# Optimization experiments

Measured on AMD Instinct MI355X. Metric: run time of the kernel, lower is better.

The kernel has to match this reference:

```python
import jax, jax.numpy as jnp
import numpy as np

B, PIX_H, PIX_W = 64, 14, 14
ENC_D, DEC_D, ATT_D, EMB_D = 2048, 512, 512, 512
VOCAB, MAX_LEN = 10000, 52  # 51 decode steps


def setup_inputs() -> dict:
    key = jax.random.key(0)
    ks = jax.random.split(key, 24)
    s = 0.02
    inp = {
        'encoder_out': jax.random.normal(ks[0], (B, PIX_H, PIX_W, ENC_D), jnp.float32),
        'encoded_captions': jax.random.randint(ks[1], (B, MAX_LEN), 0, VOCAB),
        'caption_lengths': jnp.sort(jax.random.randint(ks[2], (B,), 2, MAX_LEN + 1))[::-1].at[0].set(MAX_LEN),
        # embedding (uniform -0.1..0.1 as in init_weights)
        'emb': jax.random.uniform(ks[3], (VOCAB, EMB_D), jnp.float32, -0.1, 0.1),
        # attention network
        'W_enc_att': jax.random.normal(ks[4], (ENC_D, ATT_D)) * s,
        'b_enc_att': jnp.zeros((ATT_D,)),
        'W_dec_att': jax.random.normal(ks[5], (DEC_D, ATT_D)) * s,
        'b_dec_att': jnp.zeros((ATT_D,)),
        'W_full_att': jax.random.normal(ks[6], (ATT_D, 1)) * s,
        'b_full_att': jnp.zeros((1,)),
        # init hidden state
        'W_init_h': jax.random.normal(ks[7], (ENC_D, DEC_D)) * s,
        'b_init_h': jnp.zeros((DEC_D,)),
        'W_init_c': jax.random.normal(ks[8], (ENC_D, DEC_D)) * s,
        'b_init_c': jnp.zeros((DEC_D,)),
        # gate
        'W_fbeta': jax.random.normal(ks[9], (DEC_D, ENC_D)) * s,
        'b_fbeta': jnp.zeros((ENC_D,)),
        # LSTMCell (torch gate order i,f,g,o)
        'W_ih': jax.random.normal(ks[10], (EMB_D + ENC_D, 4 * DEC_D)) * s,
        'W_hh': jax.random.normal(ks[11], (DEC_D, 4 * DEC_D)) * s,
        'b_ih': jnp.zeros((4 * DEC_D,)),
        'b_hh': jnp.zeros((4 * DEC_D,)),
        # fc (uniform -0.1..0.1, zero bias per init_weights)
        'W_fc': jax.random.uniform(ks[12], (DEC_D, VOCAB), jnp.float32, -0.1, 0.1),
        'b_fc': jnp.zeros((VOCAB,)),
    }
    return inp


def _decode(encoder_out, encoded_captions, caption_lengths, emb,
            W_enc_att, b_enc_att, W_dec_att, b_dec_att, W_full_att, b_full_att,
            W_init_h, b_init_h, W_init_c, b_init_c, W_fbeta, b_fbeta,
            W_ih, W_hh, b_ih, b_hh, W_fc, b_fc):
    bsz = encoder_out.shape[0]
    enc = encoder_out.reshape(bsz, -1, encoder_out.shape[-1])  # [B, P, ENC_D]
    embeddings = emb[encoded_captions]                          # [B, T+1, E]
    mean_enc = enc.mean(axis=1)
    h0 = mean_enc @ W_init_h + b_init_h
    c0 = mean_enc @ W_init_c + b_init_c
    att_enc = enc @ W_enc_att + b_enc_att                       # [B, P, A] precomputed
    T = encoded_captions.shape[1] - 1                           # max decode steps
    decode_len = caption_lengths - 1                            # [B]
    step_mask = jnp.arange(T)[:, None] < decode_len[None, :]    # [T, B]
    emb_seq = jnp.swapaxes(embeddings[:, :T, :], 0, 1)          # [T, B, E]

    def step(carry, xt):
        h, c = carry
        emb_t, m = xt                                           # [B,E], [B]
        # attention: 2 linears + tanh + softmax + weighted sum
        att_dec = h @ W_dec_att + b_dec_att                     # [B, A]
        e = (jnp.tanh(att_enc + att_dec[:, None, :]) @ W_full_att + b_full_att)[..., 0]  # [B, P]
        alpha = jax.nn.softmax(e, axis=-1)
        awe = jnp.einsum('bp,bpd->bd', alpha, enc)              # [B, ENC_D]
        gate = jax.nn.sigmoid(h @ W_fbeta + b_fbeta)
        awe = gate * awe
        # LSTMCell
        x = jnp.concatenate([emb_t, awe], axis=1)
        gates = x @ W_ih + h @ W_hh + (b_ih + b_hh)
        i, f, g, o = jnp.split(gates, 4, axis=1)
        c_new = jax.nn.sigmoid(f) * c + jax.nn.sigmoid(i) * jnp.tanh(g)
        h_new = jax.nn.sigmoid(o) * jnp.tanh(c_new)
        mm = m[:, None]
        h = jnp.where(mm, h_new, h)  # freeze finished rows (== batch_size_t slicing)
        c = jnp.where(mm, c_new, c)
        preds = (h @ W_fc + b_fc) * mm  # dropout = identity (eval mode)
        return (h, c), (preds, alpha * mm)

    (_, _), (preds_seq, alpha_seq) = jax.lax.scan(step, (h0, c0), (emb_seq, step_mask))
    predictions = jnp.swapaxes(preds_seq, 0, 1)  # [B, T, V]
    alphas = jnp.swapaxes(alpha_seq, 0, 1)       # [B, T, P]
    return predictions, alphas


def reference(encoder_out, encoded_captions, caption_lengths, emb,
              W_enc_att, b_enc_att, W_dec_att, b_dec_att, W_full_att, b_full_att,
              W_init_h, b_init_h, W_init_c, b_init_c, W_fbeta, b_fbeta,
              W_ih, W_hh, b_ih, b_hh, W_fc, b_fc):
    predictions, alphas = _decode(encoder_out, encoded_captions, caption_lengths, emb,
                                  W_enc_att, b_enc_att, W_dec_att, b_dec_att, W_full_att, b_full_att,
                                  W_init_h, b_init_h, W_init_c, b_init_c, W_fbeta, b_fbeta,
                                  W_ih, W_hh, b_ih, b_hh, W_fc, b_fc)
    return predictions, encoded_captions, caption_lengths - 1, alphas
```

## Files before the change

### kernel.cpp

```cpp
#include <hip/hip_runtime.h>
#include <hip/hip_bf16.h>
#include <math.h>

#define BB 64
#define NPIX 196
#define ENCD 2048
#define DECD 512
#define VOCAB_N 10000
#define MAXLEN 52
#define TT 51
#define NPADFC 10048

#define PRED_SZ   (BB * TT * VOCAB_N)
#define CAPS_SZ   (BB * MAXLEN)
#define LENS_SZ   (BB)
#define ALPHAS_OFF (PRED_SZ + CAPS_SZ + LENS_SZ)

typedef __attribute__((ext_vector_type(8))) short short8;
typedef __attribute__((ext_vector_type(4))) short short4v;
typedef __attribute__((ext_vector_type(4))) float f32x4;

__device__ __forceinline__ float fsigm(float x) {
    return 1.0f / (1.0f + __expf(-x));
}
__device__ __forceinline__ float ftanh(float x) {
    x = fminf(fmaxf(x, -15.0f), 15.0f);
    float e = __expf(2.0f * x);
    return (e - 1.0f) / (e + 1.0f);
}
__device__ __forceinline__ float bf2f(unsigned short u) {
    union { unsigned int i; float f; } v;
    v.i = ((unsigned int)u) << 16;
    return v.f;
}
__device__ __forceinline__ unsigned short f2bf(float f) {
    union { float f; unsigned int i; } v;
    v.f = f;
    unsigned int r = v.i + 0x7FFFu + ((v.i >> 16) & 1u);
    return (unsigned short)(r >> 16);
}

__global__ __launch_bounds__(256) void gemm_mfma(
    const unsigned short* __restrict__ A, int lda,
    const unsigned short* __restrict__ Wp, int Npad,
    int nkb, long slice_stride,
    float* __restrict__ C, unsigned short* __restrict__ C16, long ldc,
    const float* __restrict__ bias, int N, int act,
    const int* __restrict__ caplen, int t)
{
    const int n0 = blockIdx.x * 64;
    const int m0 = blockIdx.y * 64;
    const int kz = blockIdx.z;
    A  += (size_t)kz * nkb * 32;
    Wp += (size_t)kz * nkb * Npad * 32;
    if (C) C += (size_t)kz * slice_stride;

    const int w  = threadIdx.x >> 6;
    const int l  = threadIdx.x & 63;
    const int lr = l & 15;
    const int q  = l >> 4;

    const unsigned short* ap = A + (size_t)(m0 + 16 * w + lr) * lda + q * 8;
    const unsigned short* bp = Wp + (size_t)(n0 + lr) * 32 + q * 8;
    const size_t bstep = (size_t)Npad * 32;

    f32x4 acc[4];
#pragma unroll
    for (int i = 0; i < 4; ++i) acc[i] = (f32x4){0.f, 0.f, 0.f, 0.f};

    short8 a  = *(const short8*)ap;
    short8 b0 = *(const short8*)(bp);
    short8 b1 = *(const short8*)(bp + 512);
    short8 b2 = *(const short8*)(bp + 1024);
    short8 b3 = *(const short8*)(bp + 1536);

    for (int kb = 0; kb < nkb; ++kb) {
        const size_t nxt = (kb + 1 < nkb) ? 1 : 0;
        const unsigned short* apn = ap + nxt * 32;
        const unsigned short* bpn = bp + nxt * bstep;
        short8 an  = *(const short8*)apn;
        short8 bn0 = *(const short8*)(bpn);
        short8 bn1 = *(const short8*)(bpn + 512);
        short8 bn2 = *(const short8*)(bpn + 1024);
        short8 bn3 = *(const short8*)(bpn + 1536);
        acc[0] = __builtin_amdgcn_mfma_f32_16x16x32_bf16(a, b0, acc[0], 0, 0, 0);
        acc[1] = __builtin_amdgcn_mfma_f32_16x16x32_bf16(a, b1, acc[1], 0, 0, 0);
        acc[2] = __builtin_amdgcn_mfma_f32_16x16x32_bf16(a, b2, acc[2], 0, 0, 0);
        acc[3] = __builtin_amdgcn_mfma_f32_16x16x32_bf16(a, b3, acc[3], 0, 0, 0);
        a = an; b0 = bn0; b1 = bn1; b2 = bn2; b3 = bn3;
        ap = apn; bp = bpn;
    }

    const int r0 = q * 4;
#pragma unroll
    for (int cf = 0; cf < 4; ++cf) {
        int col = n0 + cf * 16 + lr;
        if (col >= N) continue;
        float bv = bias ? bias[col] : 0.f;
#pragma unroll
        for (int r = 0; r < 4; ++r) {
            int row = m0 + 16 * w + r0 + r;
            float v = acc[cf][r] + bv;
            if (act == 1 || (act == 2 && col < 2048)) v = fsigm(v);
            if (caplen) v *= (t < caplen[row] - 1) ? 1.f : 0.f;
            if (C16) C16[(size_t)row * ldc + col] = f2bf(v);
            else     C [(size_t)row * ldc + col] = v;
        }
    }
}

__global__ __launch_bounds__(256) void gateslstm_kernel(
    const unsigned short* __restrict__ xcatEG,
    const unsigned short* __restrict__ hprev,
    const unsigned short* __restrict__ WpLi,
    const float* __restrict__ bsum,
    const int* __restrict__ caplen, int t,
    float* __restrict__ c,
    unsigned short* __restrict__ hnext)
{
    __shared__ float gt[4][16][68];

    const int bx = blockIdx.x;
    const int nx = bx & 31;
    const int my = bx >> 5;
    const int m0 = my * 16;
    const int n0 = nx * 64;
    const int tid = threadIdx.x;
    const int ws = tid >> 6;
    const int l  = tid & 63;
    const int lr = l & 15;
    const int q  = l >> 4;

    const unsigned short* arow_x = xcatEG + (size_t)(m0 + lr) * 2560;
    const unsigned short* arow_h = hprev  + (size_t)(m0 + lr) * 512;
    const int kbase = ws * 768 + q * 8;

    const unsigned short* bp = WpLi + ((size_t)(ws * 24) * 2048 + n0 + lr) * 32 + q * 8;
    const size_t bstep = (size_t)2048 * 32;

    f32x4 acc[4];
#pragma unroll
    for (int i = 0; i < 4; ++i) acc[i] = (f32x4){0.f, 0.f, 0.f, 0.f};

#define ALOAD(kb) ({ int k0_ = kbase + (kb) * 32; \
    (k0_ < 2560) ? *(const short8*)(arow_x + k0_) \
                 : *(const short8*)(arow_h + (k0_ - 2560)); })

    short8 a  = ALOAD(0);
    short8 b0 = *(const short8*)(bp);
    short8 b1 = *(const short8*)(bp + 512);
    short8 b2 = *(const short8*)(bp + 1024);
    short8 b3 = *(const short8*)(bp + 1536);

    for (int kb = 0; kb < 24; ++kb) {
        const int kn = (kb + 1 < 24) ? kb + 1 : kb;
        const unsigned short* bpn = bp + ((kb + 1 < 24) ? bstep : 0);
        short8 an  = ALOAD(kn);
        short8 bn0 = *(const short8*)(bpn);
        short8 bn1 = *(const short8*)(bpn + 512);
        short8 bn2 = *(const short8*)(bpn + 1024);
        short8 bn3 = *(const short8*)(bpn + 1536);
        acc[0] = __builtin_amdgcn_mfma_f32_16x16x32_bf16(a, b0, acc[0], 0, 0, 0);
        acc[1] = __builtin_amdgcn_mfma_f32_16x16x32_bf16(a, b1, acc[1], 0, 0, 0);
        acc[2] = __builtin_amdgcn_mfma_f32_16x16x32_bf16(a, b2, acc[2], 0, 0, 0);
        acc[3] = __builtin_amdgcn_mfma_f32_16x16x32_bf16(a, b3, acc[3], 0, 0, 0);
        a = an; b0 = bn0; b1 = bn1; b2 = bn2; b3 = bn3;
        bp = bpn;
    }
#undef ALOAD

    const int r0 = q * 4;
#pragma unroll
    for (int cf = 0; cf < 4; ++cf)
#pragma unroll
        for (int r = 0; r < 4; ++r)
            gt[ws][r0 + r][cf * 16 + lr] = acc[cf][r];
    __syncthreads();

    const int row = tid & 15;
    const int jj  = tid >> 4;
    const int b   = m0 + row;
    const int j   = nx * 16 + jj;
    const int lc  = 4 * jj;
    float gi = bsum[j],        gf = bsum[512 + j];
    float gg = bsum[1024 + j], go = bsum[1536 + j];
#pragma unroll
    for (int s = 0; s < 4; ++s) {
        gi += gt[s][row][lc + 0];
        gf += gt[s][row][lc + 1];
        gg += gt[s][row][lc + 2];
        go += gt[s][row][lc + 3];
    }
    const int cidx = b * 512 + j;
    float cn = fsigm(gf) * c[cidx] + fsigm(gi) * ftanh(gg);
    float hn = fsigm(go) * ftanh(cn);
    bool upd = (t < caplen[b] - 1);
    if (upd) c[cidx] = cn;
    hnext[cidx] = upd ? f2bf(hn) : hprev[cidx];
}

__global__ __launch_bounds__(512) void attawe_kernel(
    const float* __restrict__ gadec,
    const unsigned short* __restrict__ attenc16,
    const unsigned short* __restrict__ enc16,
    const float* __restrict__ Wf, const float* __restrict__ bf_,
    const float* __restrict__ emb, const int* __restrict__ caps,
    const int* __restrict__ caplen, int t,
    unsigned short* __restrict__ xcatEG,
    float* __restrict__ alphas_out)
{
    int b  = blockIdx.x & 63;
    int dh = blockIdx.x >> 6;
    int tid = threadIdx.x;
    int lane = tid & 63, wid = tid >> 6;
    __shared__ float av[512];
    __shared__ float wv[512];
    __shared__ float es[NPIX];
    __shared__ float alpha_s[NPIX];
    __shared__ float r8[8];
    __shared__ float smax, ssum;

    av[tid] = gadec[(size_t)b * 2560 + 2048 + tid];
    wv[tid] = Wf[tid];
    __syncthreads();

    float mya[8], myw[8];
#pragma unroll
    for (int i = 0; i < 8; ++i) {
        mya[i] = av[lane * 8 + i];
        myw[i] = wv[lane * 8 + i];
    }

    float bf0 = bf_[0];
    for (int p = wid; p < NPIX; p += 8) {
        const unsigned short* ae = attenc16 + ((size_t)(b * NPIX + p)) * 512 + lane * 8;
        short8 e8 = *(const short8*)ae;
        float s = 0.f;
#pragma unroll
        for (int i = 0; i < 8; ++i)
            s += ftanh(bf2f((unsigned short)e8[i]) + mya[i]) * myw[i];
        for (int off = 32; off; off >>= 1) s += __shfl_down(s, off);
        if (lane == 0) es[p] = s + bf0;
    }
    __syncthreads();

    float v = (tid < NPIX) ? es[tid] : -1e30f;
    float m = v;
    for (int off = 32; off; off >>= 1) m = fmaxf(m, __shfl_down(m, off));
    if (lane == 0) r8[wid] = m;
    __syncthreads();
    if (tid == 0) {
        float mm = r8[0];
#pragma unroll
        for (int i = 1; i < 8; ++i) mm = fmaxf(mm, r8[i]);
        smax = mm;
    }
    __syncthreads();

    float ev = (tid < NPIX) ? __expf(v - smax) : 0.0f;
    float s = ev;
    for (int off = 32; off; off >>= 1) s += __shfl_down(s, off);
    if (lane == 0) r8[wid] = s;
    __syncthreads();
    if (tid == 0) {
        float ss = 0.f;
#pragma unroll
        for (int i = 0; i < 8; ++i) ss += r8[i];
        ssum = ss;
    }
    __syncthreads();

    float mk = (t < caplen[b] - 1) ? 1.0f : 0.0f;
    if (tid < NPIX) {
        float a = ev / ssum;
        alpha_s[tid] = a;
        if (dh == 0)
            alphas_out[((size_t)b * TT + t) * NPIX + tid] = a * mk;
    }
    __syncthreads();

    unsigned short* xr = xcatEG + (size_t)b * 2560;
    int d0 = dh * 1024 + tid * 2;
    const unsigned short* e = enc16 + (size_t)b * NPIX * ENCD + d0;
    float s0 = 0.f, s1 = 0.f;
    for (int p = 0; p < NPIX; ++p) {
        unsigned int vv = *(const unsigned int*)(e + (size_t)p * ENCD);
        float a = alpha_s[p];
        s0 += a * bf2f((unsigned short)(vv & 0xffffu));
        s1 += a * bf2f((unsigned short)(vv >> 16));
    }
    const float* gtt = gadec + (size_t)b * 2560 + d0;
    xr[512 + d0 + 0] = f2bf(s0 * gtt[0]);
    xr[512 + d0 + 1] = f2bf(s1 * gtt[1]);

    if (dh == 0) {
        int wword = caps[b * MAXLEN + t];
        xr[tid] = f2bf(emb[(size_t)wword * 512 + tid]);
    }
}

__global__ __launch_bounds__(256) void preds_gemm(
    const unsigned short* __restrict__ hhist,
    const unsigned short* __restrict__ WpF,
    const float* __restrict__ bfc,
    const int* __restrict__ caplen,
    float* __restrict__ out)
{
    if (blockIdx.x >= 157) return;
    const int n0 = blockIdx.x * 64;
    const int row0 = blockIdx.y * 128;
    const bool two = (row0 + 128 <= TT * BB);
    const int w  = threadIdx.x >> 6;
    const int l  = threadIdx.x & 63;
    const int lr = l & 15;
    const int q  = l >> 4;

    const unsigned short* ap0 = hhist + (size_t)(row0 + 16 * w + lr) * 512 + q * 8;
    const unsigned short* ap1 = ap0 + (size_t)64 * 512;
    const unsigned short* bp = WpF + (size_t)(n0 + lr) * 32 + q * 8;
    const size_t bstep = (size_t)NPADFC * 32;

    f32x4 acc[4], acc2[4];
#pragma unroll
    for (int i = 0; i < 4; ++i) {
        acc[i]  = (f32x4){0.f, 0.f, 0.f, 0.f};
        acc2[i] = (f32x4){0.f, 0.f, 0.f, 0.f};
    }

    short8 a0 = *(const short8*)ap0;
    short8 a1 = two ? *(const short8*)ap1 : a0;
    short8 b0 = *(const short8*)(bp);
    short8 b1 = *(const short8*)(bp + 512);
    short8 b2 = *(const short8*)(bp + 1024);
    short8 b3 = *(const short8*)(bp + 1536);

    for (int kb = 0; kb < 16; ++kb) {
        const size_t nxt = (kb + 1 < 16) ? 1 : 0;
        const unsigned short* apn0 = ap0 + nxt * 32;
        const unsigned short* apn1 = ap1 + nxt * 32;
        const unsigned short* bpn = bp + nxt * bstep;
        short8 an0 = *(const short8*)apn0;
        short8 an1 = two ? *(const short8*)apn1 : an0;
        short8 bn0 = *(const short8*)(bpn);
        short8 bn1 = *(const short8*)(bpn + 512);
        short8 bn2 = *(const short8*)(bpn + 1024);
        short8 bn3 = *(const short8*)(bpn + 1536);
        acc[0]  = __builtin_amdgcn_mfma_f32_16x16x32_bf16(a0, b0, acc[0], 0, 0, 0);
        acc[1]  = __builtin_amdgcn_mfma_f32_16x16x32_bf16(a0, b1, acc[1], 0, 0, 0);
        acc[2]  = __builtin_amdgcn_mfma_f32_16x16x32_bf16(a0, b2, acc[2], 0, 0, 0);
        acc[3]  = __builtin_amdgcn_mfma_f32_16x16x32_bf16(a0, b3, acc[3], 0, 0, 0);
        acc2[0] = __builtin_amdgcn_mfma_f32_16x16x32_bf16(a1, b0, acc2[0], 0, 0, 0);
        acc2[1] = __builtin_amdgcn_mfma_f32_16x16x32_bf16(a1, b1, acc2[1], 0, 0, 0);
        acc2[2] = __builtin_amdgcn_mfma_f32_16x16x32_bf16(a1, b2, acc2[2], 0, 0, 0);
        acc2[3] = __builtin_amdgcn_mfma_f32_16x16x32_bf16(a1, b3, acc2[3], 0, 0, 0);
        a0 = an0; a1 = an1; b0 = bn0; b1 = bn1; b2 = bn2; b3 = bn3;
        ap0 = apn0; ap1 = apn1; bp = bpn;
    }

    const int r0 = q * 4;
#pragma unroll
    for (int cf = 0; cf < 4; ++cf) {
        int col = n0 + cf * 16 + lr;
        if (col >= VOCAB_N) continue;
        float bv = bfc[col];
#pragma unroll
        for (int r = 0; r < 4; ++r) {
            int row = row0 + 16 * w + r0 + r;
            int tt = row >> 6, b = row & 63;
            float mk = (tt < caplen[b] - 1) ? 1.f : 0.f;
            out[((size_t)b * TT + tt) * VOCAB_N + col] = (acc[cf][r] + bv) * mk;
            if (two) {
                int row2 = row + 64;
                int tt2 = row2 >> 6, b2 = row2 & 63;
                float mk2 = (tt2 < caplen[b2] - 1) ? 1.f : 0.f;
                out[((size_t)b2 * TT + tt2) * VOCAB_N + col] = (acc2[cf][r] + bv) * mk2;
            }
        }
    }
}

__global__ void pack_kernel(const float* __restrict__ W1, const float* __restrict__ W2,
                            int N1, int N2, int K1, int Npad, int mode,
                            unsigned short* __restrict__ Wp, int total)
{
    int idx = blockIdx.x * 256 + threadIdx.x;
    if (idx >= total) return;
    int kk = idx & 31;
    int r  = idx >> 5;
    int n  = r % Npad;
    int kb = r / Npad;
    int k  = kb * 32 + kk;
    float v = 0.f;
    if (mode == 0) {
        if (n < N1) v = W1[(size_t)k * N1 + n];
    } else if (mode == 1) {
        v = (n < N1) ? W1[(size_t)k * N1 + n] : W2[(size_t)k * N2 + (n - N1)];
    } else {
        v = (k < K1) ? W1[(size_t)k * N1 + n] : W2[(size_t)(k - K1) * N1 + n];
    }
    Wp[idx] = f2bf(v);
}

__global__ void packGi_kernel(const float* __restrict__ Wih,
                              const float* __restrict__ Whh,
                              unsigned short* __restrict__ Wp, int total)
{
    int idx = blockIdx.x * 256 + threadIdx.x;
    if (idx >= total) return;
    int kk = idx & 31;
    int r  = idx >> 5;
    int n  = r % 2048;
    int kb = r / 2048;
    int k  = kb * 32 + kk;
    int oc = (n & 3) * 512 + (n >> 2);
    float v = (k < 2560) ? Wih[(size_t)k * 2048 + oc]
                         : Whh[(size_t)(k - 2560) * 2048 + oc];
    Wp[idx] = f2bf(v);
}

__global__ void cast_kernel(const float* __restrict__ src,
                            unsigned short* __restrict__ dst, int n)
{
    int i = (blockIdx.x * 256 + threadIdx.x) * 4;
    if (i >= n) return;
    float4 v = *(const float4*)(src + i);
    dst[i]     = f2bf(v.x);
    dst[i + 1] = f2bf(v.y);
    dst[i + 2] = f2bf(v.z);
    dst[i + 3] = f2bf(v.w);
}

__global__ void bias_prep(const float* __restrict__ bfb, const float* __restrict__ bda,
                          const float* __restrict__ bih, const float* __restrict__ bhh,
                          const float* __restrict__ bh, const float* __restrict__ bc,
                          float* __restrict__ bcat, float* __restrict__ bsum,
                          float* __restrict__ bcatI)
{
    int i = blockIdx.x * 256 + threadIdx.x;
    if (i < 2048) { bcat[i] = bfb[i]; bsum[i] = bih[i] + bhh[i]; }
    else if (i < 2560) bcat[i] = bda[i - 2048];
    else if (i < 3072) bcatI[i - 2560] = bh[i - 2560];
    else if (i < 3584) bcatI[i - 2560] = bc[i - 3072];
}

__global__ void mean_kernel(const unsigned short* __restrict__ enc16,
                            unsigned short* __restrict__ me16)
{
    int d = blockIdx.x * 256 + threadIdx.x;
    int b = blockIdx.y;
    const unsigned short* p = enc16 + (size_t)b * NPIX * ENCD + d;
    float s = 0.0f;
    for (int q = 0; q < NPIX; ++q) s += bf2f(p[(size_t)q * ENCD]);
    me16[b * ENCD + d] = f2bf(s * (1.0f / 196.0f));
}

__global__ void inithc_fin(const float* __restrict__ hc0,
                           unsigned short* __restrict__ hh0, float* __restrict__ c)
{
    int idx = blockIdx.x * 256 + threadIdx.x;
    int b = idx >> 9, j = idx & 511;
    hh0[idx] = f2bf(hc0[(size_t)b * 1024 + j]);
    c[idx] = hc0[(size_t)b * 1024 + 512 + j];
}

__global__ void copy_misc(const int* __restrict__ caps, const int* __restrict__ lens,
                          float* __restrict__ out)
{
    int i = blockIdx.x * 256 + threadIdx.x;
    if (i < CAPS_SZ) out[PRED_SZ + i] = (float)caps[i];
    else if (i < CAPS_SZ + LENS_SZ) out[PRED_SZ + i] = (float)(lens[i - CAPS_SZ] - 1);
}

__global__ __launch_bounds__(256) void encatt_gemm(
    const unsigned short* __restrict__ A,
    const unsigned short* __restrict__ Wp,
    const float* __restrict__ bias,
    unsigned short* __restrict__ C16)
{
    const int n0 = blockIdx.x * 128;
    const int m0 = blockIdx.y * 128;
    const int w  = threadIdx.x >> 6;
    const int l  = threadIdx.x & 63;
    const int lr = l & 15;
    const int q  = l >> 4;

    const unsigned short* ap = A + (size_t)(m0 + 16 * w + lr) * 2048 + q * 8;
    const unsigned short* bp = Wp + (size_t)(n0 + lr) * 32 + q * 8;
    const size_t bstep = (size_t)512 * 32;

    f32x4 acc[16];
#pragma unroll
    for (int i = 0; i < 16; ++i) acc[i] = (f32x4){0.f, 0.f, 0.f, 0.f};

    short8 a0 = *(const short8*)(ap);
    short8 a1 = *(const short8*)(ap + 64 * 2048);
    short8 b[8];
#pragma unroll
    for (int nt = 0; nt < 8; ++nt) b[nt] = *(const short8*)(bp + nt * 512);

    for (int kb = 0; kb < 64; ++kb) {
        const size_t nxt = (kb + 1 < 64) ? 1 : 0;
        const unsigned short* apn = ap + nxt * 32;
        const unsigned short* bpn = bp + nxt * bstep;
        short8 an0 = *(const short8*)(apn);
        short8 an1 = *(const short8*)(apn + 64 * 2048);
        short8 bn[8];
#pragma unroll
        for (int nt = 0; nt < 8; ++nt) bn[nt] = *(const short8*)(bpn + nt * 512);
#pragma unroll
        for (int nt = 0; nt < 8; ++nt) {
            acc[nt]     = __builtin_amdgcn_mfma_f32_16x16x32_bf16(a0, b[nt], acc[nt], 0, 0, 0);
            acc[8 + nt] = __builtin_amdgcn_mfma_f32_16x16x32_bf16(a1, b[nt], acc[8 + nt], 0, 0, 0);
        }
        a0 = an0; a1 = an1;
#pragma unroll
        for (int nt = 0; nt < 8; ++nt) b[nt] = bn[nt];
        ap = apn; bp = bpn;
    }

    const int r0 = q * 4;
#pragma unroll
    for (int mt = 0; mt < 2; ++mt) {
#pragma unroll
        for (int nt = 0; nt < 8; ++nt) {
            int col = n0 + nt * 16 + lr;
            float bv = bias[col];
#pragma unroll
            for (int r = 0; r < 4; ++r) {
                int row = m0 + mt * 64 + 16 * w + r0 + r;
                C16[(size_t)row * 512 + col] = f2bf(acc[mt * 8 + nt][r] + bv);
            }
        }
    }
}

extern "C" void kernel_launch(void* const* d_in, const int* in_sizes, int n_in,
                              void* d_out, int out_size, void* d_ws, size_t ws_size,
                              hipStream_t stream)
{
    (void)in_sizes; (void)n_in; (void)out_size; (void)ws_size;
    const float* enc        = (const float*)d_in[0];
    const int*   caps       = (const int*)d_in[1];
    const int*   lens       = (const int*)d_in[2];
    const float* emb        = (const float*)d_in[3];
    const float* W_enc_att  = (const float*)d_in[4];
    const float* b_enc_att  = (const float*)d_in[5];
    const float* W_dec_att  = (const float*)d_in[6];
    const float* b_dec_att  = (const float*)d_in[7];
    const float* W_full_att = (const float*)d_in[8];
    const float* b_full_att = (const float*)d_in[9];
    const float* W_init_h   = (const float*)d_in[10];
    const float* b_init_h   = (const float*)d_in[11];
    const float* W_init_c   = (const float*)d_in[12];
    const float* b_init_c   = (const float*)d_in[13];
    const float* W_fbeta    = (const float*)d_in[14];
    const float* b_fbeta    = (const float*)d_in[15];
    const float* W_ih       = (const float*)d_in[16];
    const float* W_hh       = (const float*)d_in[17];
    const float* b_ih       = (const float*)d_in[18];
    const float* b_hh       = (const float*)d_in[19];
    const float* W_fc       = (const float*)d_in[20];
    const float* b_fc       = (const float*)d_in[21];
    float* out = (float*)d_out;

    char* p = (char*)d_ws;
    unsigned short* enc16   = (unsigned short*)p; p += (size_t)BB * NPIX * ENCD * 2;
    unsigned short* attenc16= (unsigned short*)p; p += (size_t)BB * NPIX * 512 * 2;
    unsigned short* WpLi    = (unsigned short*)p; p += (size_t)96 * 2048 * 32 * 2;
    unsigned short* WpG     = (unsigned short*)p; p += (size_t)16 * 2560 * 32 * 2;
    unsigned short* WpF     = (unsigned short*)p; p += (size_t)16 * NPADFC * 32 * 2;
    unsigned short* WpE     = (unsigned short*)p; p += (size_t)64 * 512 * 32 * 2;
    unsigned short* WpI     = (unsigned short*)p; p += (size_t)64 * 1024 * 32 * 2;
    unsigned short* xcatEG  = (unsigned short*)p; p += (size_t)BB * 2560 * 2;
    unsigned short* hh      = (unsigned short*)p; p += (size_t)(TT + 1) * BB * 512 * 2;
    unsigned short* me16    = (unsigned short*)p; p += (size_t)BB * ENCD * 2;
    float* gadec  = (float*)p; p += (size_t)BB * 2560 * 4;
    float* hc0    = (float*)p; p += (size_t)BB * 1024 * 4;
    float* c      = (float*)p; p += (size_t)BB * 512 * 4;
    float* bcat   = (float*)p; p += 2560 * 4;
    float* bsum   = (float*)p; p += 2048 * 4;
    float* bcatI  = (float*)p; p += 1024 * 4;

    {
        int n = BB * NPIX * ENCD;
        cast_kernel<<<(n / 4 + 255) / 256, 256, 0, stream>>>(enc, enc16, n);
    }
    { int tot = 96 * 2048 * 32;
      packGi_kernel<<<(tot + 255) / 256, 256, 0, stream>>>(W_ih, W_hh, WpLi, tot); }
    { int tot = 16 * 2560 * 32;
      pack_kernel<<<(tot + 255) / 256, 256, 0, stream>>>(W_fbeta, W_dec_att, 2048, 512, 0, 2560, 1, WpG, tot); }
    { int tot = 16 * NPADFC * 32;
      pack_kernel<<<(tot + 255) / 256, 256, 0, stream>>>(W_fc, nullptr, VOCAB_N, 0, 0, NPADFC, 0, WpF, tot); }
    { int tot = 64 * 512 * 32;
      pack_kernel<<<(tot + 255) / 256, 256, 0, stream>>>(W_enc_att, nullptr, 512, 0, 0, 512, 0, WpE, tot); }
    { int tot = 64 * 1024 * 32;
      pack_kernel<<<(tot + 255) / 256, 256, 0, stream>>>(W_init_h, W_init_c, 512, 512, 0, 1024, 1, WpI, tot); }
    bias_prep<<<14, 256, 0, stream>>>(b_fbeta, b_dec_att, b_ih, b_hh, b_init_h, b_init_c,
                                      bcat, bsum, bcatI);
    mean_kernel<<<dim3(8, 64), 256, 0, stream>>>(enc16, me16);
    gemm_mfma<<<dim3(16, 1, 1), 256, 0, stream>>>(
        me16, 2048, WpI, 1024, 64, 0, hc0, nullptr, 1024,
        bcatI, 1024, 0, nullptr, 0);
    inithc_fin<<<128, 256, 0, stream>>>(hc0, hh, c);
    encatt_gemm<<<dim3(4, 98), 256, 0, stream>>>(enc16, WpE, b_enc_att, attenc16);
    copy_misc<<<14, 256, 0, stream>>>(caps, lens, out);

    gemm_mfma<<<dim3(40, 1, 1), 256, 0, stream>>>(
        hh, 512, WpG, 2560, 16, 0, gadec, nullptr, 2560,
        bcat, 2560, 2, nullptr, 0);

    for (int t = 0; t < TT; ++t) {
        attawe_kernel<<<128, 512, 0, stream>>>(
            gadec, attenc16, enc16, W_full_att, b_full_att,
            emb, caps, lens, t, xcatEG, out + ALPHAS_OFF);
        gateslstm_kernel<<<128, 256, 0, stream>>>(
            xcatEG, hh + (size_t)t * BB * 512, WpLi, bsum, lens, t,
            c, hh + (size_t)(t + 1) * BB * 512);
        if (t + 1 < TT) {
            gemm_mfma<<<dim3(40, 1, 1), 256, 0, stream>>>(
                hh + (size_t)(t + 1) * BB * 512, 512, WpG, 2560, 16, 0,
                gadec, nullptr, 2560, bcat, 2560, 2, nullptr, 0);
        }
    }

    preds_gemm<<<dim3(160, 26), 256, 0, stream>>>(hh + (size_t)BB * 512, WpF, b_fc, lens, out);
}
```

Before: 3.130 ms.

## Fuse decoder-attention GEMM into attention kernel via flag sync; vectorize prediction stores

Merges the per-step gate/decoder-attention GEMM and the attention/weighted-encoding kernel into one launch. The first 40 blocks compute gadec and bump an atomic per-step flag, while the other 128 blocks spin on that flag before reading gadec. This removes one launch per decode step and lets the embedding gather overlap with the GEMM. It relies on all 168 blocks being co-resident to avoid deadlock. Separately, the final prediction GEMM now stages results through shared memory so it can write coalesced float4 rows instead of scattered scalar stores.

```diff
diff --git a/kernel.cpp b/kernel.cpp
--- a/kernel.cpp
+++ b/kernel.cpp
@@ -109,6 +109,182 @@
     }
 }
 
+__global__ __launch_bounds__(512) void fusedstep_kernel(
+    const unsigned short* __restrict__ hT,
+    const unsigned short* __restrict__ WpG,
+    const float* __restrict__ bcat,
+    float* __restrict__ gadec,
+    const unsigned short* __restrict__ attenc16,
+    const unsigned short* __restrict__ enc16,
+    const float* __restrict__ Wf, const float* __restrict__ bf_,
+    const float* __restrict__ emb, const int* __restrict__ caps,
+    const int* __restrict__ caplen, int t,
+    unsigned short* __restrict__ xcatEG,
+    float* __restrict__ alphas_out,
+    int* __restrict__ flag)
+{
+    const int bx = blockIdx.x;
+    const int tid = threadIdx.x;
+
+    if (bx < 40) {
+        if (tid < 256) {
+            const int n0 = bx * 64;
+            const int w  = tid >> 6;
+            const int l  = tid & 63;
+            const int lr = l & 15;
+            const int q  = l >> 4;
+
+            const unsigned short* ap = hT + (size_t)(16 * w + lr) * 512 + q * 8;
+            const unsigned short* bp = WpG + (size_t)(n0 + lr) * 32 + q * 8;
+            const size_t bstep = (size_t)2560 * 32;
+
+            f32x4 acc[4];
+#pragma unroll
+            for (int i = 0; i < 4; ++i) acc[i] = (f32x4){0.f, 0.f, 0.f, 0.f};
+
+            short8 a  = *(const short8*)ap;
+            short8 b0 = *(const short8*)(bp);
+            short8 b1 = *(const short8*)(bp + 512);
+            short8 b2 = *(const short8*)(bp + 1024);
+            short8 b3 = *(const short8*)(bp + 1536);
+
+            for (int kb = 0; kb < 16; ++kb) {
+                const size_t nxt = (kb + 1 < 16) ? 1 : 0;
+                const unsigned short* apn = ap + nxt * 32;
+                const unsigned short* bpn = bp + nxt * bstep;
+                short8 an  = *(const short8*)apn;
+                short8 bn0 = *(const short8*)(bpn);
+                short8 bn1 = *(const short8*)(bpn + 512);
+                short8 bn2 = *(const short8*)(bpn + 1024);
+                short8 bn3 = *(const short8*)(bpn + 1536);
+                acc[0] = __builtin_amdgcn_mfma_f32_16x16x32_bf16(a, b0, acc[0], 0, 0, 0);
+                acc[1] = __builtin_amdgcn_mfma_f32_16x16x32_bf16(a, b1, acc[1], 0, 0, 0);
+                acc[2] = __builtin_amdgcn_mfma_f32_16x16x32_bf16(a, b2, acc[2], 0, 0, 0);
+                acc[3] = __builtin_amdgcn_mfma_f32_16x16x32_bf16(a, b3, acc[3], 0, 0, 0);
+                a = an; b0 = bn0; b1 = bn1; b2 = bn2; b3 = bn3;
+                ap = apn; bp = bpn;
+            }
+
+            const int r0 = q * 4;
+#pragma unroll
+            for (int cf = 0; cf < 4; ++cf) {
+                int col = n0 + cf * 16 + lr;
+                float bv = bcat[col];
+#pragma unroll
+                for (int r = 0; r < 4; ++r) {
+                    int row = 16 * w + r0 + r;
+                    float v = acc[cf][r] + bv;
+                    if (col < 2048) v = fsigm(v);
+                    gadec[(size_t)row * 2560 + col] = v;
+                }
+            }
+        }
+        __syncthreads();
+        if (tid == 0) {
+            __threadfence();
+            atomicAdd(flag, 1);
+        }
+        return;
+    }
+
+    const int cb = bx - 40;
+    const int b  = cb & 63;
+    const int dh = cb >> 6;
+    const int lane = tid & 63, wid = tid >> 6;
+    __shared__ float av[512];
+    __shared__ float wv[512];
+    __shared__ float es[NPIX];
+    __shared__ float alpha_s[NPIX];
+    __shared__ float r8[8];
+    __shared__ float smax, ssum;
+
+    wv[tid] = Wf[tid];
+    unsigned short* xr = xcatEG + (size_t)b * 2560;
+    if (dh == 0) {
+        int wword = caps[b * MAXLEN + t];
+        xr[tid] = f2bf(emb[(size_t)wword * 512 + tid]);
+    }
+
+    if (tid == 0) {
+        while (__hip_atomic_load(flag, __ATOMIC_ACQUIRE, __HIP_MEMORY_SCOPE_AGENT) < 40) {
+            __builtin_amdgcn_s_sleep(1);
+        }
+        __threadfence();
+    }
+    __syncthreads();
+
+    av[tid] = gadec[(size_t)b * 2560 + 2048 + tid];
+    __syncthreads();
+
+    float mya[8], myw[8];
+#pragma unroll
+    for (int i = 0; i < 8; ++i) {
+        mya[i] = av[lane * 8 + i];
+        myw[i] = wv[lane * 8 + i];
+    }
+
+    float bf0 = bf_[0];
+    for (int p = wid; p < NPIX; p += 8) {
+        const unsigned short* ae = attenc16 + ((size_t)(b * NPIX + p)) * 512 + lane * 8;
+        short8 e8 = *(const short8*)ae;
+        float s = 0.f;
+#pragma unroll
+        for (int i = 0; i < 8; ++i)
+            s += ftanh(bf2f((unsigned short)e8[i]) + mya[i]) * myw[i];
+        for (int off = 32; off; off >>= 1) s += __shfl_down(s, off);
+        if (lane == 0) es[p] = s + bf0;
+    }
+    __syncthreads();
+
+    float v = (tid < NPIX) ? es[tid] : -1e30f;
+    float m = v;
+    for (int off = 32; off; off >>= 1) m = fmaxf(m, __shfl_down(m, off));
+    if (lane == 0) r8[wid] = m;
+    __syncthreads();
+    if (tid == 0) {
+        float mm = r8[0];
+#pragma unroll
+        for (int i = 1; i < 8; ++i) mm = fmaxf(mm, r8[i]);
+        smax = mm;
+    }
+    __syncthreads();
+
+    float ev = (tid < NPIX) ? __expf(v - smax) : 0.0f;
+    float s = ev;
+    for (int off = 32; off; off >>= 1) s += __shfl_down(s, off);
+    if (lane == 0) r8[wid] = s;
+    __syncthreads();
+    if (tid == 0) {
+        float ss = 0.f;
+#pragma unroll
+        for (int i = 0; i < 8; ++i) ss += r8[i];
+        ssum = ss;
+    }
+    __syncthreads();
+
+    float mk = (t < caplen[b] - 1) ? 1.0f : 0.0f;
+    if (tid < NPIX) {
+        float a = ev / ssum;
+        alpha_s[tid] = a;
+        if (dh == 0)
+            alphas_out[((size_t)b * TT + t) * NPIX + tid] = a * mk;
+    }
+    __syncthreads();
+
+    int d0 = dh * 1024 + tid * 2;
+    const unsigned short* e = enc16 + (size_t)b * NPIX * ENCD + d0;
+    float s0 = 0.f, s1 = 0.f;
+    for (int p = 0; p < NPIX; ++p) {
+        unsigned int vv = *(const unsigned int*)(e + (size_t)p * ENCD);
+        float a = alpha_s[p];
+        s0 += a * bf2f((unsigned short)(vv & 0xffffu));
+        s1 += a * bf2f((unsigned short)(vv >> 16));
+    }
+    const float* gtt = gadec + (size_t)b * 2560 + d0;
+    xr[512 + d0 + 0] = f2bf(s0 * gtt[0]);
+    xr[512 + d0 + 1] = f2bf(s1 * gtt[1]);
+}
+
 __global__ __launch_bounds__(256) void gateslstm_kernel(
     const unsigned short* __restrict__ xcatEG,
     const unsigned short* __restrict__ hprev,
@@ -199,106 +375,6 @@
     hnext[cidx] = upd ? f2bf(hn) : hprev[cidx];
 }
 
-__global__ __launch_bounds__(512) void attawe_kernel(
-    const float* __restrict__ gadec,
-    const unsigned short* __restrict__ attenc16,
-    const unsigned short* __restrict__ enc16,
-    const float* __restrict__ Wf, const float* __restrict__ bf_,
-    const float* __restrict__ emb, const int* __restrict__ caps,
-    const int* __restrict__ caplen, int t,
-    unsigned short* __restrict__ xcatEG,
-    float* __restrict__ alphas_out)
-{
-    int b  = blockIdx.x & 63;
-    int dh = blockIdx.x >> 6;
-    int tid = threadIdx.x;
-    int lane = tid & 63, wid = tid >> 6;
-    __shared__ float av[512];
-    __shared__ float wv[512];
-    __shared__ float es[NPIX];
-    __shared__ float alpha_s[NPIX];
-    __shared__ float r8[8];
-    __shared__ float smax, ssum;
-
-    av[tid] = gadec[(size_t)b * 2560 + 2048 + tid];
-    wv[tid] = Wf[tid];
-    __syncthreads();
-
-    float mya[8], myw[8];
-#pragma unroll
-    for (int i = 0; i < 8; ++i) {
-        mya[i] = av[lane * 8 + i];
-        myw[i] = wv[lane * 8 + i];
-    }
-
-    float bf0 = bf_[0];
-    for (int p = wid; p < NPIX; p += 8) {
-        const unsigned short* ae = attenc16 + ((size_t)(b * NPIX + p)) * 512 + lane * 8;
-        short8 e8 = *(const short8*)ae;
-        float s = 0.f;
-#pragma unroll
-        for (int i = 0; i < 8; ++i)
-            s += ftanh(bf2f((unsigned short)e8[i]) + mya[i]) * myw[i];
-        for (int off = 32; off; off >>= 1) s += __shfl_down(s, off);
-        if (lane == 0) es[p] = s + bf0;
-    }
-    __syncthreads();
-
-    float v = (tid < NPIX) ? es[tid] : -1e30f;
-    float m = v;
-    for (int off = 32; off; off >>= 1) m = fmaxf(m, __shfl_down(m, off));
-    if (lane == 0) r8[wid] = m;
-    __syncthreads();
-    if (tid == 0) {
-        float mm = r8[0];
-#pragma unroll
-        for (int i = 1; i < 8; ++i) mm = fmaxf(mm, r8[i]);
-        smax = mm;
-    }
-    __syncthreads();
-
-    float ev = (tid < NPIX) ? __expf(v - smax) : 0.0f;
-    float s = ev;
-    for (int off = 32; off; off >>= 1) s += __shfl_down(s, off);
-    if (lane == 0) r8[wid] = s;
-    __syncthreads();
-    if (tid == 0) {
-        float ss = 0.f;
-#pragma unroll
-        for (int i = 0; i < 8; ++i) ss += r8[i];
-        ssum = ss;
-    }
-    __syncthreads();
-
-    float mk = (t < caplen[b] - 1) ? 1.0f : 0.0f;
-    if (tid < NPIX) {
-        float a = ev / ssum;
-        alpha_s[tid] = a;
-        if (dh == 0)
-            alphas_out[((size_t)b * TT + t) * NPIX + tid] = a * mk;
-    }
-    __syncthreads();
-
-    unsigned short* xr = xcatEG + (size_t)b * 2560;
-    int d0 = dh * 1024 + tid * 2;
-    const unsigned short* e = enc16 + (size_t)b * NPIX * ENCD + d0;
-    float s0 = 0.f, s1 = 0.f;
-    for (int p = 0; p < NPIX; ++p) {
-        unsigned int vv = *(const unsigned int*)(e + (size_t)p * ENCD);
-        float a = alpha_s[p];
-        s0 += a * bf2f((unsigned short)(vv & 0xffffu));
-        s1 += a * bf2f((unsigned short)(vv >> 16));
-    }
-    const float* gtt = gadec + (size_t)b * 2560 + d0;
-    xr[512 + d0 + 0] = f2bf(s0 * gtt[0]);
-    xr[512 + d0 + 1] = f2bf(s1 * gtt[1]);
-
-    if (dh == 0) {
-        int wword = caps[b * MAXLEN + t];
-        xr[tid] = f2bf(emb[(size_t)wword * 512 + tid]);
-    }
-}
-
 __global__ __launch_bounds__(256) void preds_gemm(
     const unsigned short* __restrict__ hhist,
     const unsigned short* __restrict__ WpF,
@@ -307,6 +383,7 @@
     float* __restrict__ out)
 {
     if (blockIdx.x >= 157) return;
+    __shared__ float ot[64][68];
     const int n0 = blockIdx.x * 64;
     const int row0 = blockIdx.y * 128;
     const bool two = (row0 + 128 <= TT * BB);
@@ -358,24 +435,42 @@
     }
 
     const int r0 = q * 4;
-#pragma unroll
-    for (int cf = 0; cf < 4; ++cf) {
-        int col = n0 + cf * 16 + lr;
-        if (col >= VOCAB_N) continue;
-        float bv = bfc[col];
-#pragma unroll
-        for (int r = 0; r < 4; ++r) {
-            int row = row0 + 16 * w + r0 + r;
+    const int colg = threadIdx.x & 15;
+    const int rowi = threadIdx.x >> 4;
+    const int cbase = n0 + colg * 4;
+
+#pragma unroll
+    for (int mt = 0; mt < 2; ++mt) {
+        if (mt == 1 && !two) break;
+#pragma unroll
+        for (int cf = 0; cf < 4; ++cf)
+#pragma unroll
+            for (int r = 0; r < 4; ++r)
+                ot[16 * w + r0 + r][cf * 16 + lr] = mt ? acc2[cf][r] : acc[cf][r];
+        __syncthreads();
+
+#pragma unroll
+        for (int ps = 0; ps < 4; ++ps) {
+            int lrow = ps * 16 + rowi;
+            int row = row0 + mt * 64 + lrow;
             int tt = row >> 6, b = row & 63;
             float mk = (tt < caplen[b] - 1) ? 1.f : 0.f;
-            out[((size_t)b * TT + tt) * VOCAB_N + col] = (acc[cf][r] + bv) * mk;
-            if (two) {
-                int row2 = row + 64;
-                int tt2 = row2 >> 6, b2 = row2 & 63;
-                float mk2 = (tt2 < caplen[b2] - 1) ? 1.f : 0.f;
-                out[((size_t)b2 * TT + tt2) * VOCAB_N + col] = (acc2[cf][r] + bv) * mk2;
+            float4 v;
+            v.x = (ot[lrow][colg * 4 + 0] + bfc[cbase + 0]) * mk;
+            v.y = (ot[lrow][colg * 4 + 1] + bfc[cbase + 1]) * mk;
+            v.z = (ot[lrow][colg * 4 + 2] + bfc[cbase + 2]) * mk;
+            v.w = (ot[lrow][colg * 4 + 3] + bfc[cbase + 3]) * mk;
+            float* o = out + ((size_t)b * TT + tt) * VOCAB_N + cbase;
+            if (cbase + 3 < VOCAB_N) {
+                *(float4*)o = v;
+            } else {
+                if (cbase + 0 < VOCAB_N) o[0] = v.x;
+                if (cbase + 1 < VOCAB_N) o[1] = v.y;
+                if (cbase + 2 < VOCAB_N) o[2] = v.z;
+                if (cbase + 3 < VOCAB_N) o[3] = v.w;
             }
         }
+        __syncthreads();
     }
 }
 
@@ -434,13 +529,14 @@
                           const float* __restrict__ bih, const float* __restrict__ bhh,
                           const float* __restrict__ bh, const float* __restrict__ bc,
                           float* __restrict__ bcat, float* __restrict__ bsum,
-                          float* __restrict__ bcatI)
+                          float* __restrict__ bcatI, int* __restrict__ flags)
 {
     int i = blockIdx.x * 256 + threadIdx.x;
     if (i < 2048) { bcat[i] = bfb[i]; bsum[i] = bih[i] + bhh[i]; }
     else if (i < 2560) bcat[i] = bda[i - 2048];
     else if (i < 3072) bcatI[i - 2560] = bh[i - 2560];
     else if (i < 3584) bcatI[i - 2560] = bc[i - 3072];
+    else if (i < 3648) flags[i - 3584] = 0;
 }
 
 __global__ void mean_kernel(const unsigned short* __restrict__ enc16,
@@ -580,6 +676,7 @@
     float* bcat   = (float*)p; p += 2560 * 4;
     float* bsum   = (float*)p; p += 2048 * 4;
     float* bcatI  = (float*)p; p += 1024 * 4;
+    int*   flags  = (int*)p;  p += 64 * 4;
 
     {
         int n = BB * NPIX * ENCD;
@@ -595,8 +692,8 @@
       pack_kernel<<<(tot + 255) / 256, 256, 0, stream>>>(W_enc_att, nullptr, 512, 0, 0, 512, 0, WpE, tot); }
     { int tot = 64 * 1024 * 32;
       pack_kernel<<<(tot + 255) / 256, 256, 0, stream>>>(W_init_h, W_init_c, 512, 512, 0, 1024, 1, WpI, tot); }
-    bias_prep<<<14, 256, 0, stream>>>(b_fbeta, b_dec_att, b_ih, b_hh, b_init_h, b_init_c,
-                                      bcat, bsum, bcatI);
+    bias_prep<<<15, 256, 0, stream>>>(b_fbeta, b_dec_att, b_ih, b_hh, b_init_h, b_init_c,
+                                      bcat, bsum, bcatI, flags);
     mean_kernel<<<dim3(8, 64), 256, 0, stream>>>(enc16, me16);
     gemm_mfma<<<dim3(16, 1, 1), 256, 0, stream>>>(
         me16, 2048, WpI, 1024, 64, 0, hc0, nullptr, 1024,
@@ -605,22 +702,14 @@
     encatt_gemm<<<dim3(4, 98), 256, 0, stream>>>(enc16, WpE, b_enc_att, attenc16);
     copy_misc<<<14, 256, 0, stream>>>(caps, lens, out);
 
-    gemm_mfma<<<dim3(40, 1, 1), 256, 0, stream>>>(
-        hh, 512, WpG, 2560, 16, 0, gadec, nullptr, 2560,
-        bcat, 2560, 2, nullptr, 0);
-
     for (int t = 0; t < TT; ++t) {
-        attawe_kernel<<<128, 512, 0, stream>>>(
-            gadec, attenc16, enc16, W_full_att, b_full_att,
-            emb, caps, lens, t, xcatEG, out + ALPHAS_OFF);
+        fusedstep_kernel<<<168, 512, 0, stream>>>(
+            hh + (size_t)t * BB * 512, WpG, bcat, gadec,
+            attenc16, enc16, W_full_att, b_full_att,
+            emb, caps, lens, t, xcatEG, out + ALPHAS_OFF, flags + t);
         gateslstm_kernel<<<128, 256, 0, stream>>>(
             xcatEG, hh + (size_t)t * BB * 512, WpLi, bsum, lens, t,
             c, hh + (size_t)(t + 1) * BB * 512);
-        if (t + 1 < TT) {
-            gemm_mfma<<<dim3(40, 1, 1), 256, 0, stream>>>(
-                hh + (size_t)(t + 1) * BB * 512, 512, WpG, 2560, 16, 0,
-                gadec, nullptr, 2560, bcat, 2560, 2, nullptr, 0);
-        }
     }
 
     preds_gemm<<<dim3(160, 26), 256, 0, stream>>>(hh + (size_t)BB * 512, WpF, b_fc, lens, out);
```

New measurement: 4.388 ms. 40.2% more time.
